# Kernel tuning notes

Measured on AMD Instinct MI355X. Metric: run time of the kernel, lower is better.

The kernel has to match this reference:

```python
import jax, jax.numpy as jnp
import numpy as np
from functools import partial

B, T, D, H, HL, L, C = 64, 1024, 256, 256, 256, 2, 128


def _rnn_layer(x, Wih, Whh, bih, bhh):
    # x: [B, T, D] -> outputs [B, T, H]; torch nn.RNN (tanh) semantics
    proj = jnp.einsum('btd,hd->bth', x, Wih) + bih + bhh  # precompute input projection
    h0 = jnp.zeros((x.shape[0], Whh.shape[0]), x.dtype)

    def step(h, p_t):
        h = jnp.tanh(p_t + h @ Whh.T)
        return h, h

    _, ys = jax.lax.scan(step, h0, proj.swapaxes(0, 1))  # scan over time [T, B, H]
    return ys.swapaxes(0, 1)


def _lstm_layer(x, Wih, Whh, bih, bhh):
    # torch nn.LSTM gate order: i, f, g, o. Wih: [4H, D], Whh: [4H, H]
    Hh = Whh.shape[1]
    proj = jnp.einsum('btd,gd->btg', x, Wih) + bih + bhh  # [B, T, 4H]
    h0 = jnp.zeros((x.shape[0], Hh), x.dtype)
    c0 = jnp.zeros((x.shape[0], Hh), x.dtype)

    def step(carry, p_t):
        h, c = carry
        gates = p_t + h @ Whh.T
        i, f, g, o = jnp.split(gates, 4, axis=-1)
        i = jax.nn.sigmoid(i)
        f = jax.nn.sigmoid(f)
        g = jnp.tanh(g)
        o = jax.nn.sigmoid(o)
        c = f * c + i * g
        h = o * jnp.tanh(c)
        return (h, c), h

    _, ys = jax.lax.scan(step, (h0, c0), proj.swapaxes(0, 1))
    return ys.swapaxes(0, 1)


def setup_inputs() -> dict:
    key = jax.random.key(0)
    ks = jax.random.split(key, 12)
    s = 1.0 / np.sqrt(H)
    return {
        'rnn_x': jax.random.normal(ks[0], (B, T, D), jnp.float32),
        'lstm_x': jax.random.normal(ks[1], (B, T, D), jnp.float32),
        'rnn_Wih': jax.random.normal(ks[2], (L, H, D), jnp.float32) * s,
        'rnn_Whh': jax.random.normal(ks[3], (L, H, H), jnp.float32) * s,
        'rnn_bih': jax.random.normal(ks[4], (L, H), jnp.float32) * s,
        'rnn_bhh': jax.random.normal(ks[5], (L, H), jnp.float32) * s,
        'lstm_Wih': jax.random.normal(ks[6], (L, 4 * HL, D), jnp.float32) * s,
        'lstm_Whh': jax.random.normal(ks[7], (L, 4 * HL, HL), jnp.float32) * s,
        'lstm_bih': jax.random.normal(ks[8], (L, 4 * HL), jnp.float32) * s,
        'lstm_bhh': jax.random.normal(ks[9], (L, 4 * HL), jnp.float32) * s,
        'fc_W': jax.random.normal(ks[10], (C, H + HL), jnp.float32) * (1.0 / np.sqrt(H + HL)),
        'fc_b': jax.random.normal(ks[11], (C,), jnp.float32) * (1.0 / np.sqrt(H + HL)),
    }


def reference(rnn_x, lstm_x, rnn_Wih, rnn_Whh, rnn_bih, rnn_bhh,
              lstm_Wih, lstm_Whh, lstm_bih, lstm_bhh, fc_W, fc_b):
    r = rnn_x
    for l in range(L):
        r = _rnn_layer(r, rnn_Wih[l], rnn_Whh[l], rnn_bih[l], rnn_bhh[l])
    m = lstm_x
    for l in range(L):
        m = _lstm_layer(m, lstm_Wih[l], lstm_Whh[l], lstm_bih[l], lstm_bhh[l])
    feat = jnp.concatenate([r[:, -1, :], m[:, -1, :]], axis=1)  # [B, H+HL]
    return feat @ fc_W.T + fc_b
```

## Files before the change

kernel.cpp:

```cpp
#include <hip/hip_runtime.h>
#include <stdint.h>

#define T_ 1024

typedef short bf16x8 __attribute__((ext_vector_type(8)));
typedef float f32x4  __attribute__((ext_vector_type(4)));
typedef unsigned short u16;

#define MFMA(a,b,c) __builtin_amdgcn_mfma_f32_16x16x32_bf16((a),(b),(c),0,0,0)

__device__ __forceinline__ u16 f2bf(float f){
  unsigned u = __float_as_uint(f);
  return (u16)((u + 0x7FFFu + ((u>>16)&1u)) >> 16);
}
__device__ __forceinline__ float bf2f(u16 s){ return __uint_as_float(((unsigned)s)<<16); }
__device__ __forceinline__ float sigm(float x){ return 1.f/(1.f+__expf(-x)); }
__device__ __forceinline__ float tanhq(float x){ return 2.f/(1.f+__expf(-2.f*x)) - 1.f; }

__device__ __forceinline__ void gload16(const void* g, void* l){
  __builtin_amdgcn_global_load_lds(
      (const __attribute__((address_space(1))) unsigned int*)g,
      (__attribute__((address_space(3)))       unsigned int*)l, 16, 0, 0);
}
__device__ __forceinline__ void lgkm0_barrier(){
  asm volatile("s_waitcnt lgkmcnt(0)" ::: "memory");
  __builtin_amdgcn_s_barrier();
  asm volatile("" ::: "memory");
}

__global__ void k_cvt(const float* __restrict__ s, u16* __restrict__ d, int n4){
  int i = blockIdx.x*blockDim.x + threadIdx.x;
  int stride = gridDim.x*blockDim.x;
  for (; i < n4; i += stride){
    float4 v = ((const float4*)s)[i];
    ushort4 o; o.x=f2bf(v.x); o.y=f2bf(v.y); o.z=f2bf(v.z); o.w=f2bf(v.w);
    ((ushort4*)d)[i] = o;
  }
}

__global__ __launch_bounds__(256,2) void k_gemm(
    const u16* __restrict__ A, const u16* __restrict__ Bm,
    u16* __restrict__ C, int N)
{
  __shared__ u16 As[128*64];
  __shared__ u16 Bs[128*64];
  const int tid = threadIdx.x;
  const int lane = tid & 63, w = tid >> 6;
  const int l15 = lane & 15, l4 = lane >> 4;
  const long m0 = (long)blockIdx.x * 128;
  const int  n0 = blockIdx.y * 128;
  const int  mo = (w>>1)*64, no = (w&1)*64;

  f32x4 acc[4][4];
  #pragma unroll
  for (int i=0;i<4;++i)
    #pragma unroll
    for (int j=0;j<4;++j) acc[i][j] = (f32x4){0.f,0.f,0.f,0.f};

  for (int kt=0; kt<4; ++kt){
    const int k0 = kt*64;
    #pragma unroll
    for (int i=0;i<4;++i){
      int fb = (i*256+tid)*16;
      int r  = fb>>7, cbyte = fb&127;
      gload16(A + (m0 + r)*256 + k0 + (cbyte>>1), (char*)As + fb);
      gload16(Bm + (long)(n0 + r)*256 + k0 + (cbyte>>1), (char*)Bs + fb);
    }
    __syncthreads();
    #pragma unroll
    for (int kb=0;kb<2;++kb){
      bf16x8 a[4], b[4];
      #pragma unroll
      for (int mb=0;mb<4;++mb)
        a[mb] = *(const bf16x8*)(As + (mo+mb*16+l15)*64 + kb*32 + l4*8);
      #pragma unroll
      for (int nb=0;nb<4;++nb)
        b[nb] = *(const bf16x8*)(Bs + (no+nb*16+l15)*64 + kb*32 + l4*8);
      #pragma unroll
      for (int mb=0;mb<4;++mb)
        #pragma unroll
        for (int nb=0;nb<4;++nb)
          acc[mb][nb] = MFMA(a[mb], b[nb], acc[mb][nb]);
    }
    __syncthreads();
  }
  #pragma unroll
  for (int mb=0;mb<4;++mb)
    #pragma unroll
    for (int nb=0;nb<4;++nb)
      #pragma unroll
      for (int j=0;j<4;++j){
        long row = m0 + mo + mb*16 + l4*4 + j;
        int  col = n0 + no + nb*16 + l15;
        C[row*N + col] = f2bf(acc[mb][nb][j]);
      }
}

__global__ __launch_bounds__(512,2) void k_rec(
    const u16*  __restrict__ projR,
    const float* __restrict__ WhhR,
    const float* __restrict__ bihR, const float* __restrict__ bhhR,
    u16* __restrict__ yR,
    const u16*  __restrict__ projL,
    const float* __restrict__ WhhL,
    const float* __restrict__ bihL, const float* __restrict__ bhhL,
    u16* __restrict__ yL,
    u16* __restrict__ hbuf,
    int* __restrict__ flags,
    float* __restrict__ feat,
    int lastMode)
{
  __shared__ u16 hlds[16*256];
  const int tid = threadIdx.x;
  const int lane = tid & 63, w = tid >> 6;
  const int l15 = lane & 15, l4 = lane >> 4, l7 = lane & 7;
  const int bid = blockIdx.x;

  if (bid < 4){
    const int g = bid;
    const int cb = 32*w;
    bf16x8 bhi[2][8], blo[2][8];
    #pragma unroll
    for (int nb=0;nb<2;++nb){
      const int col = cb + nb*16 + l15;
      #pragma unroll
      for (int kb=0;kb<8;++kb){
        const float* wp = WhhR + (long)col*256 + kb*32 + l4*8;
        #pragma unroll
        for (int j=0;j<8;++j){
          float wv = wp[j];
          u16 hi = f2bf(wv);
          bhi[nb][kb][j] = (short)hi;
          blo[nb][kb][j] = (short)f2bf(wv - bf2f(hi));
        }
      }
    }
    float bias[2];
    #pragma unroll
    for (int nb=0;nb<2;++nb){ int col = cb+nb*16+l15; bias[nb]=bihR[col]+bhhR[col]; }

    u16 pfr[8];
    #pragma unroll
    for (int nb=0;nb<2;++nb)
      #pragma unroll
      for (int j=0;j<4;++j)
        pfr[nb*4+j] = projR[((long)(16*g + l4*4 + j)*T_ + 0)*256 + cb + nb*16 + l15];

    for (int t=0; t<T_; ++t){
      lgkm0_barrier();
      f32x4 acc0 = {0.f,0.f,0.f,0.f}, acc1 = acc0;
      if (t > 0){
        bf16x8 a[8];
        #pragma unroll
        for (int kb=0;kb<8;++kb){
          int bo = (l15*512 + kb*64 + l4*16) ^ ((l15&7)<<4);
          a[kb] = *(const bf16x8*)((const char*)hlds + bo);
        }
        #pragma unroll
        for (int kb=0;kb<8;++kb){
          acc0 = MFMA(a[kb], bhi[0][kb], acc0);
          acc0 = MFMA(a[kb], blo[0][kb], acc0);
          acc1 = MFMA(a[kb], bhi[1][kb], acc1);
          acc1 = MFMA(a[kb], blo[1][kb], acc1);
        }
      }
      float hv[2][4];
      #pragma unroll
      for (int nb=0;nb<2;++nb)
        #pragma unroll
        for (int j=0;j<4;++j){
          float pre = (nb ? acc1[j] : acc0[j]) + bf2f(pfr[nb*4+j]) + bias[nb];
          hv[nb][j] = tanhq(pre);
        }
      int tn = (t+1 < T_) ? t+1 : t;
      #pragma unroll
      for (int nb=0;nb<2;++nb)
        #pragma unroll
        for (int j=0;j<4;++j)
          pfr[nb*4+j] = projR[((long)(16*g + l4*4 + j)*T_ + tn)*256 + cb + nb*16 + l15];
      lgkm0_barrier();
      #pragma unroll
      for (int nb=0;nb<2;++nb)
        #pragma unroll
        for (int j=0;j<4;++j){
          int m = l4*4 + j, u = cb + nb*16 + l15;
          u16 hb = f2bf(hv[nb][j]);
          int bo = (m*512 + u*2) ^ ((m&7)<<4);
          *(u16*)((char*)hlds + bo) = hb;
          if (yR) yR[((long)(16*g+m)*T_ + t)*256 + u] = hb;
          if (lastMode && t == T_-1) feat[(16*g+m)*512 + u] = hv[nb][j];
        }
    }
  } else {
    const int wg = bid - 4;
    const int bg = wg >> 2, hg = wg & 3;
    const int ub = 64*hg + 8*w;
    const int ugl = ub + l7;
    bf16x8 bhi[2][8], blo[2][8];
    float bias[2];
    #pragma unroll
    for (int nb=0;nb<2;++nb){
      const int gate = nb*2 + (l15>>3);
      const long wr = (long)(gate*256 + ub + l7);
      bias[nb] = bihL[wr] + bhhL[wr];
      #pragma unroll
      for (int kb=0;kb<8;++kb){
        const float* wp = WhhL + wr*256 + kb*32 + l4*8;
        #pragma unroll
        for (int j=0;j<8;++j){
          float wv = wp[j];
          u16 hi = f2bf(wv);
          bhi[nb][kb][j] = (short)hi;
          blo[nb][kb][j] = (short)f2bf(wv - bf2f(hi));
        }
      }
    }
    u16 pfr[8];
    #pragma unroll
    for (int nb=0;nb<2;++nb){
      const int gate = nb*2 + (l15>>3);
      #pragma unroll
      for (int j=0;j<4;++j)
        pfr[nb*4+j] = projL[((long)(16*bg + l4*4 + j)*T_ + 0)*1024 + gate*256 + ub + l7];
    }
    float c4[4] = {0.f,0.f,0.f,0.f};
    const bool lowHalf = ((lane & 8) == 0);

    for (int t=0; t<T_; ++t){
      const int par = t & 1, pn = par ^ 1;
      if (t > 0 && tid == 0){
        while (__hip_atomic_load(flags + bg, __ATOMIC_RELAXED, __HIP_MEMORY_SCOPE_AGENT) < 4*t)
          __builtin_amdgcn_s_sleep(1);
        __threadfence();
      }
      lgkm0_barrier();
      f32x4 acc0 = {0.f,0.f,0.f,0.f}, acc1 = acc0;
      if (t > 0){
        bf16x8 a[8];
        const u16* hb = hbuf + par*16384 + (16*bg + l15)*256;
        #pragma unroll
        for (int kb=0;kb<8;++kb) a[kb] = *(const bf16x8*)(hb + kb*32 + l4*8);
        #pragma unroll
        for (int kb=0;kb<8;++kb){
          acc0 = MFMA(a[kb], bhi[0][kb], acc0);
          acc0 = MFMA(a[kb], blo[0][kb], acc0);
          acc1 = MFMA(a[kb], bhi[1][kb], acc1);
          acc1 = MFMA(a[kb], blo[1][kb], acc1);
        }
      }
      #pragma unroll
      for (int j=0;j<4;++j){
        float s0 = acc0[j] + bf2f(pfr[j])   + bias[0];
        float s1 = acc1[j] + bf2f(pfr[4+j]) + bias[1];
        float g0 = sigm(s0);
        float g1 = lowHalf ? tanhq(s1) : sigm(s1);
        float p0 = __shfl_xor(g0, 8);
        float p1 = __shfl_xor(g1, 8);
        float iv = lowHalf ? g0 : p0;
        float fv = lowHalf ? p0 : g0;
        float gv = lowHalf ? g1 : p1;
        float ov = lowHalf ? p1 : g1;
        float cv = fv * c4[j] + iv * gv;
        c4[j] = cv;
        float hval = ov * tanhq(cv);
        int m = l4*4 + j;
        if (lowHalf){
          u16 hb2 = f2bf(hval);
          hbuf[pn*16384 + (16*bg+m)*256 + ugl] = hb2;
          if (yL) yL[((long)(16*bg+m)*T_ + t)*256 + ugl] = hb2;
          if (lastMode && t == T_-1) feat[(16*bg+m)*512 + 256 + ugl] = hval;
        }
      }
      int tn = (t+1 < T_) ? t+1 : t;
      #pragma unroll
      for (int nb=0;nb<2;++nb){
        const int gate = nb*2 + (l15>>3);
        #pragma unroll
        for (int j=0;j<4;++j)
          pfr[nb*4+j] = projL[((long)(16*bg + l4*4 + j)*T_ + tn)*1024 + gate*256 + ub + l7];
      }
      asm volatile("s_waitcnt vmcnt(8)" ::: "memory");
      __builtin_amdgcn_s_barrier();
      asm volatile("" ::: "memory");
      if (tid == 0){ __threadfence(); atomicAdd(flags + bg, 1); }
    }
  }
}

__global__ void k_fc(const float* __restrict__ feat, const float* __restrict__ W,
                     const float* __restrict__ bias, float* __restrict__ out){
  int o = blockIdx.x*blockDim.x + threadIdx.x;
  if (o >= 64*128) return;
  int b = o >> 7, c = o & 127;
  float s = bias[c];
  const float* f  = feat + b*512;
  const float* wr = W + c*512;
  #pragma unroll 8
  for (int k=0;k<512;++k) s += f[k]*wr[k];
  out[o] = s;
}

extern "C" void kernel_launch(void* const* d_in, const int* in_sizes, int n_in,
                              void* d_out, int out_size, void* d_ws, size_t ws_size,
                              hipStream_t stream)
{
  (void)in_sizes; (void)n_in; (void)out_size; (void)ws_size;
  const float* rnn_x    = (const float*)d_in[0];
  const float* lstm_x   = (const float*)d_in[1];
  const float* rnn_Wih  = (const float*)d_in[2];
  const float* rnn_Whh  = (const float*)d_in[3];
  const float* rnn_bih  = (const float*)d_in[4];
  const float* rnn_bhh  = (const float*)d_in[5];
  const float* lstm_Wih = (const float*)d_in[6];
  const float* lstm_Whh = (const float*)d_in[7];
  const float* lstm_bih = (const float*)d_in[8];
  const float* lstm_bhh = (const float*)d_in[9];
  const float* fc_W     = (const float*)d_in[10];
  const float* fc_b     = (const float*)d_in[11];
  float* out = (float*)d_out;

  char* ws = (char*)d_ws; size_t off = 0;
  auto alloc = [&](size_t b)->char*{ char* p = ws + off; off += (b + 255) & ~(size_t)255; return p; };
  const size_t NE = (size_t)64*1024*256;
  u16*  wih_r = (u16*)alloc(2*256*256*2);
  u16*  wih_l = (u16*)alloc(2*1024*256*2);
  u16*  xr    = (u16*)alloc(NE*2);
  u16*  xl    = (u16*)alloc(NE*2);
  u16*  projR = (u16*)alloc(NE*2);
  u16*  projL = (u16*)alloc(NE*4*2);
  u16*  hbuf  = (u16*)alloc(2*64*256*2);
  int*  flags = (int*)alloc(256);
  float* feat = (float*)alloc(64*512*4);

  hipMemsetAsync(flags, 0, 256, stream);
  k_cvt<<<2048,256,0,stream>>>(rnn_x,  xr, (int)(NE/4));
  k_cvt<<<2048,256,0,stream>>>(lstm_x, xl, (int)(NE/4));
  k_cvt<<<64, 256,0,stream>>>(rnn_Wih,  wih_r, 2*256*256/4);
  k_cvt<<<256,256,0,stream>>>(lstm_Wih, wih_l, 2*1024*256/4);
  k_gemm<<<dim3(512,2),256,0,stream>>>(xr, wih_r, projR, 256);
  k_gemm<<<dim3(512,8),256,0,stream>>>(xl, wih_l, projL, 1024);
  k_rec<<<20,512,0,stream>>>(projR, rnn_Whh, rnn_bih, rnn_bhh, xr,
                             projL, lstm_Whh, lstm_bih, lstm_bhh, xl,
                             hbuf, flags, nullptr, 0);
  k_gemm<<<dim3(512,2),256,0,stream>>>(xr, wih_r + 256*256,  projR, 256);
  k_gemm<<<dim3(512,8),256,0,stream>>>(xl, wih_l + 1024*256, projL, 1024);
  k_rec<<<20,512,0,stream>>>(projR, rnn_Whh + 256*256, rnn_bih + 256, rnn_bhh + 256, nullptr,
                             projL, lstm_Whh + 1024*256, lstm_bih + 1024, lstm_bhh + 1024, nullptr,
                             hbuf, flags + 32, feat, 1);
  k_fc<<<32,256,0,stream>>>(feat, fc_W, fc_b, out);
}
```

Measured before the change: 10.69 ms.

## Shrink LSTM recurrence to four blocks with per-wave flags and cache-bypass loads

The LSTM part of the recurrent kernel now uses 4 workgroups, one per hidden slice, and each walks all four batch groups instead of using one workgroup per batch/hidden pair. The block-wide barrier plus atomic counter is replaced with per-wave flag words written and polled through coherent (sc0 sc1) global stores and loads. Loads of the next batch group's h fragments are overlapped with the MFMAs of the current one. The aim is to cut the number of participants in each step's cross-block handshake and the barrier cost, at the price of more serial work per block and hand-written waitcnt ordering that is fragile.

```diff
diff --git a/kernel.cpp b/kernel.cpp
--- a/kernel.cpp
+++ b/kernel.cpp
@@ -27,6 +27,32 @@
   __builtin_amdgcn_s_barrier();
   asm volatile("" ::: "memory");
 }
+
+__device__ __forceinline__ int coh_ld32(const int* p){
+  int r;
+  asm volatile("global_load_dword %0, %1, off sc0 sc1\n\ts_waitcnt vmcnt(0)"
+               : "=v"(r) : "v"(p) : "memory");
+  return r;
+}
+__device__ __forceinline__ void coh_st32(int* p, int v){
+  asm volatile("global_store_dword %0, %1, off sc0 sc1" :: "v"(p), "v"(v) : "memory");
+}
+__device__ __forceinline__ void coh_st16(u16* p, u16 v){
+  unsigned vv = v;
+  asm volatile("global_store_short %0, %1, off sc0 sc1" :: "v"(p), "v"(vv) : "memory");
+}
+__device__ __forceinline__ void coh_ld_frags(const u16* base, bf16x8 a[8]){
+  asm volatile("global_load_dwordx4 %0, %1, off sc0 sc1"            : "=v"(a[0]) : "v"(base) : "memory");
+  asm volatile("global_load_dwordx4 %0, %1, off offset:64 sc0 sc1"  : "=v"(a[1]) : "v"(base) : "memory");
+  asm volatile("global_load_dwordx4 %0, %1, off offset:128 sc0 sc1" : "=v"(a[2]) : "v"(base) : "memory");
+  asm volatile("global_load_dwordx4 %0, %1, off offset:192 sc0 sc1" : "=v"(a[3]) : "v"(base) : "memory");
+  asm volatile("global_load_dwordx4 %0, %1, off offset:256 sc0 sc1" : "=v"(a[4]) : "v"(base) : "memory");
+  asm volatile("global_load_dwordx4 %0, %1, off offset:320 sc0 sc1" : "=v"(a[5]) : "v"(base) : "memory");
+  asm volatile("global_load_dwordx4 %0, %1, off offset:384 sc0 sc1" : "=v"(a[6]) : "v"(base) : "memory");
+  asm volatile("global_load_dwordx4 %0, %1, off offset:448 sc0 sc1" : "=v"(a[7]) : "v"(base) : "memory");
+}
+#define VMCNT(n) do{ asm volatile("s_waitcnt vmcnt(" #n ")" ::: "memory"); \
+                     __builtin_amdgcn_sched_barrier(0); }while(0)
 
 __global__ void k_cvt(const float* __restrict__ s, u16* __restrict__ d, int n4){
   int i = blockIdx.x*blockDim.x + threadIdx.x;
@@ -115,6 +141,7 @@
   const int lane = tid & 63, w = tid >> 6;
   const int l15 = lane & 15, l4 = lane >> 4, l7 = lane & 7;
   const int bid = blockIdx.x;
+  (void)lastMode;
 
   if (bid < 4){
     const int g = bid;
@@ -188,12 +215,11 @@
           int bo = (m*512 + u*2) ^ ((m&7)<<4);
           *(u16*)((char*)hlds + bo) = hb;
           if (yR) yR[((long)(16*g+m)*T_ + t)*256 + u] = hb;
-          if (lastMode && t == T_-1) feat[(16*g+m)*512 + u] = hv[nb][j];
+          if (feat && t == T_-1) feat[(16*g+m)*512 + u] = hv[nb][j];
         }
     }
   } else {
-    const int wg = bid - 4;
-    const int bg = wg >> 2, hg = wg & 3;
+    const int hg = bid - 4;
     const int ub = 64*hg + 8*w;
     const int ugl = ub + l7;
     bf16x8 bhi[2][8], blo[2][8];
@@ -201,7 +227,7 @@
     #pragma unroll
     for (int nb=0;nb<2;++nb){
       const int gate = nb*2 + (l15>>3);
-      const long wr = (long)(gate*256 + ub + l7);
+      const long wr = (long)(gate*256 + ugl);
       bias[nb] = bihL[wr] + bhhL[wr];
       #pragma unroll
       for (int kb=0;kb<8;++kb){
@@ -215,74 +241,83 @@
         }
       }
     }
-    u16 pfr[8];
-    #pragma unroll
-    for (int nb=0;nb<2;++nb){
-      const int gate = nb*2 + (l15>>3);
-      #pragma unroll
-      for (int j=0;j<4;++j)
-        pfr[nb*4+j] = projL[((long)(16*bg + l4*4 + j)*T_ + 0)*1024 + gate*256 + ub + l7];
-    }
-    float c4[4] = {0.f,0.f,0.f,0.f};
+    u16 pfr[4][8];
+    #pragma unroll
+    for (int bg=0;bg<4;++bg)
+      #pragma unroll
+      for (int nb=0;nb<2;++nb){
+        const int gate = nb*2 + (l15>>3);
+        #pragma unroll
+        for (int j=0;j<4;++j)
+          pfr[bg][nb*4+j] = projL[((long)(16*bg + l4*4 + j)*T_ + 0)*1024 + gate*256 + ugl];
+      }
+    float cst[4][4];
+    #pragma unroll
+    for (int bg=0;bg<4;++bg){ cst[bg][0]=0.f;cst[bg][1]=0.f;cst[bg][2]=0.f;cst[bg][3]=0.f; }
     const bool lowHalf = ((lane & 8) == 0);
+    int* flg = flags;
 
     for (int t=0; t<T_; ++t){
       const int par = t & 1, pn = par ^ 1;
-      if (t > 0 && tid == 0){
-        while (__hip_atomic_load(flags + bg, __ATOMIC_RELAXED, __HIP_MEMORY_SCOPE_AGENT) < 4*t)
-          __builtin_amdgcn_s_sleep(1);
-        __threadfence();
-      }
-      lgkm0_barrier();
-      f32x4 acc0 = {0.f,0.f,0.f,0.f}, acc1 = acc0;
+      bf16x8 afr[8];
       if (t > 0){
-        bf16x8 a[8];
-        const u16* hb = hbuf + par*16384 + (16*bg + l15)*256;
-        #pragma unroll
-        for (int kb=0;kb<8;++kb) a[kb] = *(const bf16x8*)(hb + kb*32 + l4*8);
-        #pragma unroll
-        for (int kb=0;kb<8;++kb){
-          acc0 = MFMA(a[kb], bhi[0][kb], acc0);
-          acc0 = MFMA(a[kb], blo[0][kb], acc0);
-          acc1 = MFMA(a[kb], bhi[1][kb], acc1);
-          acc1 = MFMA(a[kb], blo[1][kb], acc1);
-        }
-      }
-      #pragma unroll
-      for (int j=0;j<4;++j){
-        float s0 = acc0[j] + bf2f(pfr[j])   + bias[0];
-        float s1 = acc1[j] + bf2f(pfr[4+j]) + bias[1];
-        float g0 = sigm(s0);
-        float g1 = lowHalf ? tanhq(s1) : sigm(s1);
-        float p0 = __shfl_xor(g0, 8);
-        float p1 = __shfl_xor(g1, 8);
-        float iv = lowHalf ? g0 : p0;
-        float fv = lowHalf ? p0 : g0;
-        float gv = lowHalf ? g1 : p1;
-        float ov = lowHalf ? p1 : g1;
-        float cv = fv * c4[j] + iv * gv;
-        c4[j] = cv;
-        float hval = ov * tanhq(cv);
-        int m = l4*4 + j;
-        if (lowHalf){
-          u16 hb2 = f2bf(hval);
-          hbuf[pn*16384 + (16*bg+m)*256 + ugl] = hb2;
-          if (yL) yL[((long)(16*bg+m)*T_ + t)*256 + ugl] = hb2;
-          if (lastMode && t == T_-1) feat[(16*bg+m)*512 + 256 + ugl] = hval;
-        }
-      }
-      int tn = (t+1 < T_) ? t+1 : t;
-      #pragma unroll
-      for (int nb=0;nb<2;++nb){
-        const int gate = nb*2 + (l15>>3);
-        #pragma unroll
-        for (int j=0;j<4;++j)
-          pfr[nb*4+j] = projL[((long)(16*bg + l4*4 + j)*T_ + tn)*1024 + gate*256 + ub + l7];
+        while (true){
+          int a0 = coh_ld32(flg + lane);
+          int a1 = coh_ld32(flg + 64 + lane);
+          if (__all((a0 >= t) & (a1 >= t))) break;
+          __builtin_amdgcn_s_sleep(2);
+        }
+        coh_ld_frags(hbuf + par*16384 + l15*256 + l4*8, afr);
+      }
+      #pragma unroll
+      for (int bg=0;bg<4;++bg){
+        f32x4 acc0={0.f,0.f,0.f,0.f}, acc1={0.f,0.f,0.f,0.f};
+        if (t > 0){
+          if (bg == 0){ VMCNT(0); } else { VMCNT(12); }
+          #pragma unroll
+          for (int kb=0;kb<8;++kb){
+            acc0 = MFMA(afr[kb], bhi[0][kb], acc0);
+            acc0 = MFMA(afr[kb], blo[0][kb], acc0);
+            acc1 = MFMA(afr[kb], bhi[1][kb], acc1);
+            acc1 = MFMA(afr[kb], blo[1][kb], acc1);
+          }
+          if (bg < 3)
+            coh_ld_frags(hbuf + par*16384 + (16*(bg+1)+l15)*256 + l4*8, afr);
+        }
+        #pragma unroll
+        for (int j=0;j<4;++j){
+          float s0 = acc0[j] + bf2f(pfr[bg][j])   + bias[0];
+          float s1 = acc1[j] + bf2f(pfr[bg][4+j]) + bias[1];
+          float g0 = sigm(s0);
+          float g1 = lowHalf ? tanhq(s1) : sigm(s1);
+          float p0 = __shfl_xor(g0, 8);
+          float p1 = __shfl_xor(g1, 8);
+          float iv = lowHalf ? g0 : p0;
+          float fv = lowHalf ? p0 : g0;
+          float gv = lowHalf ? g1 : p1;
+          float ov = lowHalf ? p1 : g1;
+          float cv = fv * cst[bg][j] + iv * gv;
+          cst[bg][j] = cv;
+          float hval = ov * tanhq(cv);
+          const int m = 16*bg + l4*4 + j;
+          if (lowHalf){
+            u16 hb2 = f2bf(hval);
+            coh_st16(hbuf + pn*16384 + m*256 + ugl, hb2);
+            if (yL) yL[((long)m*T_ + t)*256 + ugl] = hb2;
+            if (feat && t == T_-1) feat[m*512 + 256 + ugl] = hval;
+          }
+        }
+        const int tn = (t+1 < T_) ? t+1 : t;
+        #pragma unroll
+        for (int nb=0;nb<2;++nb){
+          const int gate = nb*2 + (l15>>3);
+          #pragma unroll
+          for (int j=0;j<4;++j)
+            pfr[bg][nb*4+j] = projL[((long)(16*bg + l4*4 + j)*T_ + tn)*1024 + gate*256 + ugl];
+        }
       }
       asm volatile("s_waitcnt vmcnt(8)" ::: "memory");
-      __builtin_amdgcn_s_barrier();
-      asm volatile("" ::: "memory");
-      if (tid == 0){ __threadfence(); atomicAdd(flags + bg, 1); }
+      if (lane < 4) coh_st32(flg + lane*32 + hg*8 + w, t+1);
     }
   }
 }
@@ -329,23 +364,23 @@
   u16*  projR = (u16*)alloc(NE*2);
   u16*  projL = (u16*)alloc(NE*4*2);
   u16*  hbuf  = (u16*)alloc(2*64*256*2);
-  int*  flags = (int*)alloc(256);
+  int*  flags = (int*)alloc(1024);
   float* feat = (float*)alloc(64*512*4);
 
-  hipMemsetAsync(flags, 0, 256, stream);
+  hipMemsetAsync(flags, 0, 1024, stream);
   k_cvt<<<2048,256,0,stream>>>(rnn_x,  xr, (int)(NE/4));
   k_cvt<<<2048,256,0,stream>>>(lstm_x, xl, (int)(NE/4));
   k_cvt<<<64, 256,0,stream>>>(rnn_Wih,  wih_r, 2*256*256/4);
   k_cvt<<<256,256,0,stream>>>(lstm_Wih, wih_l, 2*1024*256/4);
   k_gemm<<<dim3(512,2),256,0,stream>>>(xr, wih_r, projR, 256);
   k_gemm<<<dim3(512,8),256,0,stream>>>(xl, wih_l, projL, 1024);
-  k_rec<<<20,512,0,stream>>>(projR, rnn_Whh, rnn_bih, rnn_bhh, xr,
-                             projL, lstm_Whh, lstm_bih, lstm_bhh, xl,
-                             hbuf, flags, nullptr, 0);
+  k_rec<<<8,512,0,stream>>>(projR, rnn_Whh, rnn_bih, rnn_bhh, xr,
+                            projL, lstm_Whh, lstm_bih, lstm_bhh, xl,
+                            hbuf, flags, nullptr, 0);
   k_gemm<<<dim3(512,2),256,0,stream>>>(xr, wih_r + 256*256,  projR, 256);
   k_gemm<<<dim3(512,8),256,0,stream>>>(xl, wih_l + 1024*256, projL, 1024);
-  k_rec<<<20,512,0,stream>>>(projR, rnn_Whh + 256*256, rnn_bih + 256, rnn_bhh + 256, nullptr,
-                             projL, lstm_Whh + 1024*256, lstm_bih + 1024, lstm_bhh + 1024, nullptr,
-                             hbuf, flags + 32, feat, 1);
+  k_rec<<<8,512,0,stream>>>(projR, rnn_Whh + 256*256, rnn_bih + 256, rnn_bhh + 256, nullptr,
+                            projL, lstm_Whh + 1024*256, lstm_bih + 1024, lstm_bhh + 1024, nullptr,
+                            hbuf, flags + 128, feat, 1);
   k_fc<<<32,256,0,stream>>>(feat, fc_W, fc_b, out);
 }
```

After: 36.53 ms. 242% more time.

## Replace LSTM atomic flag sync with tagged h-buffer polling and batch-interleaved pipeline

Applied to the files above, without the earlier changes.

The LSTM recurrence shrinks from 16 to 4 workgroups. Each workgroup now owns a hidden-unit slice for all four batch groups and interleaves them so one group's exchange latency hides behind another group's compute. The atomic counter barrier is replaced by a tag (layer, batch group, timestep) packed into the upper half of each h word. Consumers poll with uncached loads until the tags match. The GEMM output layout changes to time-major so per-step projection reads are contiguous. This trades fewer global round-trips for more work per workgroup and depends on the polling being correct.

```diff
diff --git a/kernel.cpp b/kernel.cpp
--- a/kernel.cpp
+++ b/kernel.cpp
@@ -5,6 +5,7 @@
 
 typedef short bf16x8 __attribute__((ext_vector_type(8)));
 typedef float f32x4  __attribute__((ext_vector_type(4)));
+typedef int   i32x4  __attribute__((ext_vector_type(4)));
 typedef unsigned short u16;
 
 #define MFMA(a,b,c) __builtin_amdgcn_mfma_f32_16x16x32_bf16((a),(b),(c),0,0,0)
@@ -27,6 +28,12 @@
   __builtin_amdgcn_s_barrier();
   asm volatile("" ::: "memory");
 }
+
+#define VMCNT(n) do{ asm volatile("s_waitcnt vmcnt(" #n ")" ::: "memory"); \
+                     __builtin_amdgcn_sched_barrier(0); }while(0)
+#define LD_X4(dst, p, OFF) asm volatile("global_load_dwordx4 %0, %1, off offset:" #OFF " sc0 sc1" : "=v"(dst) : "v"(p) : "memory")
+#define ST_TAG(p, v)       asm volatile("global_store_dword %0, %1, off sc0 sc1" :: "v"(p), "v"(v) : "memory")
+#define LD_U16(dst, p, OFF) asm volatile("global_load_ushort %0, %1, off offset:" #OFF : "=v"(dst) : "v"(p) : "memory")
 
 __global__ void k_cvt(const float* __restrict__ s, u16* __restrict__ d, int n4){
   int i = blockIdx.x*blockDim.x + threadIdx.x;
@@ -90,9 +97,10 @@
     for (int nb=0;nb<4;++nb)
       #pragma unroll
       for (int j=0;j<4;++j){
-        long row = m0 + mo + mb*16 + l4*4 + j;
+        long m   = m0 + mo + mb*16 + l4*4 + j;
+        long crow= (long)(m & 1023)*64 + (m >> 10);
         int  col = n0 + no + nb*16 + l15;
-        C[row*N + col] = f2bf(acc[mb][nb][j]);
+        C[crow*N + col] = f2bf(acc[mb][nb][j]);
       }
 }
 
@@ -105,12 +113,12 @@
     const float* __restrict__ WhhL,
     const float* __restrict__ bihL, const float* __restrict__ bhhL,
     u16* __restrict__ yL,
-    u16* __restrict__ hbuf,
-    int* __restrict__ flags,
+    unsigned* __restrict__ hbuf,
     float* __restrict__ feat,
-    int lastMode)
+    int lay)
 {
   __shared__ u16 hlds[16*256];
+  __shared__ u16 lsm[2*16*256];
   const int tid = threadIdx.x;
   const int lane = tid & 63, w = tid >> 6;
   const int l15 = lane & 15, l4 = lane >> 4, l7 = lane & 7;
@@ -144,7 +152,7 @@
     for (int nb=0;nb<2;++nb)
       #pragma unroll
       for (int j=0;j<4;++j)
-        pfr[nb*4+j] = projR[((long)(16*g + l4*4 + j)*T_ + 0)*256 + cb + nb*16 + l15];
+        pfr[nb*4+j] = projR[(long)(0*64 + 16*g + l4*4 + j)*256 + cb + nb*16 + l15];
 
     for (int t=0; t<T_; ++t){
       lgkm0_barrier();
@@ -177,7 +185,7 @@
       for (int nb=0;nb<2;++nb)
         #pragma unroll
         for (int j=0;j<4;++j)
-          pfr[nb*4+j] = projR[((long)(16*g + l4*4 + j)*T_ + tn)*256 + cb + nb*16 + l15];
+          pfr[nb*4+j] = projR[(long)(tn*64 + 16*g + l4*4 + j)*256 + cb + nb*16 + l15];
       lgkm0_barrier();
       #pragma unroll
       for (int nb=0;nb<2;++nb)
@@ -188,20 +196,25 @@
           int bo = (m*512 + u*2) ^ ((m&7)<<4);
           *(u16*)((char*)hlds + bo) = hb;
           if (yR) yR[((long)(16*g+m)*T_ + t)*256 + u] = hb;
-          if (lastMode && t == T_-1) feat[(16*g+m)*512 + u] = hv[nb][j];
+          if (feat && t == T_-1) feat[(16*g+m)*512 + u] = hv[nb][j];
         }
     }
   } else {
-    const int wg = bid - 4;
-    const int bg = wg >> 2, hg = wg & 3;
+    const int hg = bid - 4;
     const int ub = 64*hg + 8*w;
     const int ugl = ub + l7;
+    const int srow  = 2*w + (lane>>5);
+    const int scol8 = (lane&31)*8;
+    const int swro  = ((srow*512 + (lane&31)*16) ^ ((srow&7)<<4));
+    char* lsmBE = (char*)lsm;
+    char* lsmBO = (char*)lsm + 8192;
+
     bf16x8 bhi[2][8], blo[2][8];
     float bias[2];
     #pragma unroll
     for (int nb=0;nb<2;++nb){
       const int gate = nb*2 + (l15>>3);
-      const long wr = (long)(gate*256 + ub + l7);
+      const long wr = (long)(gate*256 + ugl);
       bias[nb] = bihL[wr] + bhhL[wr];
       #pragma unroll
       for (int kb=0;kb<8;++kb){
@@ -215,75 +228,115 @@
         }
       }
     }
-    u16 pfr[8];
-    #pragma unroll
-    for (int nb=0;nb<2;++nb){
-      const int gate = nb*2 + (l15>>3);
-      #pragma unroll
-      for (int j=0;j<4;++j)
-        pfr[nb*4+j] = projL[((long)(16*bg + l4*4 + j)*T_ + 0)*1024 + gate*256 + ub + l7];
-    }
-    float c4[4] = {0.f,0.f,0.f,0.f};
+    float cst[4][4];
+    #pragma unroll
+    for (int b_=0;b_<4;++b_){ cst[b_][0]=0.f;cst[b_][1]=0.f;cst[b_][2]=0.f;cst[b_][3]=0.f; }
     const bool lowHalf = ((lane & 8) == 0);
-
-    for (int t=0; t<T_; ++t){
-      const int par = t & 1, pn = par ^ 1;
-      if (t > 0 && tid == 0){
-        while (__hip_atomic_load(flags + bg, __ATOMIC_RELAXED, __HIP_MEMORY_SCOPE_AGENT) < 4*t)
-          __builtin_amdgcn_s_sleep(1);
-        __threadfence();
-      }
-      lgkm0_barrier();
-      f32x4 acc0 = {0.f,0.f,0.f,0.f}, acc1 = acc0;
-      if (t > 0){
-        bf16x8 a[8];
-        const u16* hb = hbuf + par*16384 + (16*bg + l15)*256;
-        #pragma unroll
-        for (int kb=0;kb<8;++kb) a[kb] = *(const bf16x8*)(hb + kb*32 + l4*8);
-        #pragma unroll
-        for (int kb=0;kb<8;++kb){
-          acc0 = MFMA(a[kb], bhi[0][kb], acc0);
-          acc0 = MFMA(a[kb], blo[0][kb], acc0);
-          acc1 = MFMA(a[kb], bhi[1][kb], acc1);
-          acc1 = MFMA(a[kb], blo[1][kb], acc1);
-        }
-      }
-      #pragma unroll
-      for (int j=0;j<4;++j){
-        float s0 = acc0[j] + bf2f(pfr[j])   + bias[0];
-        float s1 = acc1[j] + bf2f(pfr[4+j]) + bias[1];
-        float g0 = sigm(s0);
-        float g1 = lowHalf ? tanhq(s1) : sigm(s1);
-        float p0 = __shfl_xor(g0, 8);
-        float p1 = __shfl_xor(g1, 8);
-        float iv = lowHalf ? g0 : p0;
-        float fv = lowHalf ? p0 : g0;
-        float gv = lowHalf ? g1 : p1;
-        float ov = lowHalf ? p1 : g1;
-        float cv = fv * c4[j] + iv * gv;
-        c4[j] = cv;
-        float hval = ov * tanhq(cv);
-        int m = l4*4 + j;
-        if (lowHalf){
-          u16 hb2 = f2bf(hval);
-          hbuf[pn*16384 + (16*bg+m)*256 + ugl] = hb2;
-          if (yL) yL[((long)(16*bg+m)*T_ + t)*256 + ugl] = hb2;
-          if (lastMode && t == T_-1) feat[(16*bg+m)*512 + 256 + ugl] = hval;
-        }
-      }
-      int tn = (t+1 < T_) ? t+1 : t;
-      #pragma unroll
-      for (int nb=0;nb<2;++nb){
-        const int gate = nb*2 + (l15>>3);
-        #pragma unroll
-        for (int j=0;j<4;++j)
-          pfr[nb*4+j] = projL[((long)(16*bg + l4*4 + j)*T_ + tn)*1024 + gate*256 + ub + l7];
-      }
-      asm volatile("s_waitcnt vmcnt(8)" ::: "memory");
-      __builtin_amdgcn_s_barrier();
-      asm volatile("" ::: "memory");
-      if (tid == 0){ __threadfence(); atomicAdd(flags + bg, 1); }
-    }
+    i32x4 rE0, rE1, rO0, rO1;
+    unsigned pfE[8], pfO[8];
+
+    #define PFR_ISSUE(PF, TP, BGP) do{                                             \
+      const u16* pb  = projL + ((size_t)((TP)*64 + 16*(BGP) + l4*4)*1024 + (l15>>3)*256 + ugl); \
+      const u16* pb2 = pb + 2048;                                                  \
+      LD_U16(PF[0], pb, 0);    LD_U16(PF[4], pb, 1024);                            \
+      LD_U16(PF[1], pb, 2048); LD_U16(PF[5], pb, 3072);                            \
+      LD_U16(PF[2], pb2, 0);    LD_U16(PF[6], pb2, 1024);                          \
+      LD_U16(PF[3], pb2, 2048); LD_U16(PF[7], pb2, 3072);                          \
+    }while(0)
+
+    #define STAGE_ISSUE(R0, R1, T2, BG2) do{                                       \
+      const unsigned* sp = hbuf + ((T2)&1)*16384 + (16*(BG2) + srow)*256 + scol8;  \
+      LD_X4(R0, sp, 0); LD_X4(R1, sp, 16);                                         \
+    }while(0)
+
+    #define LACT(BG, PF, TT) do{                                                   \
+      const unsigned tws = (unsigned)(((lay<<13)|((BG)<<11)|((TT)+1))<<16);        \
+      unsigned* hstb = hbuf + (((TT)&1)^1)*16384 + (16*(BG) + l4*4)*256 + ugl;     \
+      _Pragma("unroll")                                                            \
+      for (int j=0;j<4;++j){                                                       \
+        float s0v = acc0[j] + bf2f((u16)PF[j])   + bias[0];                        \
+        float s1v = acc1[j] + bf2f((u16)PF[4+j]) + bias[1];                        \
+        float g0 = sigm(s0v);                                                      \
+        float g1 = lowHalf ? tanhq(s1v) : sigm(s1v);                               \
+        float p0 = __shfl_xor(g0, 8);                                              \
+        float p1 = __shfl_xor(g1, 8);                                              \
+        float iv = lowHalf ? g0 : p0;                                              \
+        float fv = lowHalf ? p0 : g0;                                              \
+        float gv = lowHalf ? g1 : p1;                                              \
+        float ov = lowHalf ? p1 : g1;                                              \
+        float cv = fv * cst[BG][j] + iv * gv;                                      \
+        cst[BG][j] = cv;                                                           \
+        float hval = ov * tanhq(cv);                                               \
+        if (lowHalf){                                                              \
+          u16 hb2 = f2bf(hval);                                                    \
+          unsigned dw = tws | (unsigned)hb2;                                       \
+          ST_TAG(hstb + j*256, dw);                                                \
+          yL[((long)(16*(BG) + l4*4 + j)*T_ + (TT))*256 + ugl] = hb2;              \
+          if (feat && (TT) == T_-1) feat[(16*(BG)+l4*4+j)*512 + 256 + ugl] = hval; \
+        }                                                                          \
+      }                                                                            \
+    }while(0)
+
+    PFR_ISSUE(pfE, 0, 0);
+    PFR_ISSUE(pfO, 0, 1);
+    VMCNT(0);
+    {
+      f32x4 acc0 = {0.f,0.f,0.f,0.f}, acc1 = {0.f,0.f,0.f,0.f};
+      LACT(0, pfE, 0); PFR_ISSUE(pfE, 0, 2);
+      LACT(1, pfO, 0); PFR_ISSUE(pfO, 0, 3);
+      STAGE_ISSUE(rE0, rE1, 1, 0); VMCNT(0);
+      LACT(2, pfE, 0); PFR_ISSUE(pfE, 1, 0);
+      STAGE_ISSUE(rO0, rO1, 1, 1); VMCNT(0);
+      LACT(3, pfO, 0); PFR_ISSUE(pfO, 1, 1);
+    }
+
+    #define LSLOT(BG, R0, R1, PF, LSB) do{                                         \
+      VMCNT(34);                                                                   \
+      {                                                                            \
+        const unsigned tw = (unsigned)(((lay<<13)|((BG)<<11)|t)<<16);              \
+        for(;;){                                                                   \
+          unsigned bad;                                                            \
+          bad  = (unsigned)(R0[0]^(int)tw)&0xFFFF0000u;                            \
+          bad |= (unsigned)(R0[1]^(int)tw)&0xFFFF0000u;                            \
+          bad |= (unsigned)(R0[2]^(int)tw)&0xFFFF0000u;                            \
+          bad |= (unsigned)(R0[3]^(int)tw)&0xFFFF0000u;                            \
+          bad |= (unsigned)(R1[0]^(int)tw)&0xFFFF0000u;                            \
+          bad |= (unsigned)(R1[1]^(int)tw)&0xFFFF0000u;                            \
+          bad |= (unsigned)(R1[2]^(int)tw)&0xFFFF0000u;                            \
+          bad |= (unsigned)(R1[3]^(int)tw)&0xFFFF0000u;                            \
+          if (!__any(bad != 0u)) break;                                            \
+          STAGE_ISSUE(R0, R1, t, BG); VMCNT(0);                                    \
+        }                                                                          \
+        i32x4 pk;                                                                  \
+        pk[0]=(int)__builtin_amdgcn_perm((unsigned)R0[1],(unsigned)R0[0],0x05040100u); \
+        pk[1]=(int)__builtin_amdgcn_perm((unsigned)R0[3],(unsigned)R0[2],0x05040100u); \
+        pk[2]=(int)__builtin_amdgcn_perm((unsigned)R1[1],(unsigned)R1[0],0x05040100u); \
+        pk[3]=(int)__builtin_amdgcn_perm((unsigned)R1[3],(unsigned)R1[2],0x05040100u); \
+        *(i32x4*)(lsmB##LSB + swro) = pk;                                          \
+      }                                                                            \
+      { int t2 = t + ((BG)>=2 ? 1:0); if (t2 > T_-1) t2 = T_-1;                    \
+        STAGE_ISSUE(R0, R1, t2, ((BG)+2)&3); }                                     \
+      lgkm0_barrier();                                                             \
+      f32x4 acc0 = {0.f,0.f,0.f,0.f}, acc1 = {0.f,0.f,0.f,0.f};                    \
+      _Pragma("unroll")                                                            \
+      for (int kb=0;kb<8;++kb){                                                    \
+        bf16x8 a = *(const bf16x8*)(lsmB##LSB + ((l15*512 + kb*64 + l4*16) ^ ((l15&7)<<4))); \
+        acc0 = MFMA(a, bhi[0][kb], acc0);  acc0 = MFMA(a, blo[0][kb], acc0);       \
+        acc1 = MFMA(a, bhi[1][kb], acc1);  acc1 = MFMA(a, blo[1][kb], acc1);       \
+      }                                                                            \
+      VMCNT(20);                                                                   \
+      LACT(BG, PF, t);                                                             \
+      { int tp = t + ((BG)>=2 ? 1:0); if (tp > T_-1) tp = T_-1;                    \
+        PFR_ISSUE(PF, tp, ((BG)+2)&3); }                                           \
+    }while(0)
+
+    for (int t=1; t<T_; ++t){
+      LSLOT(0, rE0, rE1, pfE, E);
+      LSLOT(1, rO0, rO1, pfO, O);
+      LSLOT(2, rE0, rE1, pfE, E);
+      LSLOT(3, rO0, rO1, pfO, O);
+    }
+    VMCNT(0);
   }
 }
 
@@ -328,24 +381,22 @@
   u16*  xl    = (u16*)alloc(NE*2);
   u16*  projR = (u16*)alloc(NE*2);
   u16*  projL = (u16*)alloc(NE*4*2);
-  u16*  hbuf  = (u16*)alloc(2*64*256*2);
-  int*  flags = (int*)alloc(256);
+  unsigned* hbuf = (unsigned*)alloc(2*64*256*4);
   float* feat = (float*)alloc(64*512*4);
 
-  hipMemsetAsync(flags, 0, 256, stream);
   k_cvt<<<2048,256,0,stream>>>(rnn_x,  xr, (int)(NE/4));
   k_cvt<<<2048,256,0,stream>>>(lstm_x, xl, (int)(NE/4));
   k_cvt<<<64, 256,0,stream>>>(rnn_Wih,  wih_r, 2*256*256/4);
   k_cvt<<<256,256,0,stream>>>(lstm_Wih, wih_l, 2*1024*256/4);
   k_gemm<<<dim3(512,2),256,0,stream>>>(xr, wih_r, projR, 256);
   k_gemm<<<dim3(512,8),256,0,stream>>>(xl, wih_l, projL, 1024);
-  k_rec<<<20,512,0,stream>>>(projR, rnn_Whh, rnn_bih, rnn_bhh, xr,
-                             projL, lstm_Whh, lstm_bih, lstm_bhh, xl,
-                             hbuf, flags, nullptr, 0);
+  k_rec<<<8,512,0,stream>>>(projR, rnn_Whh, rnn_bih, rnn_bhh, xr,
+                            projL, lstm_Whh, lstm_bih, lstm_bhh, xl,
+                            hbuf, nullptr, 0);
   k_gemm<<<dim3(512,2),256,0,stream>>>(xr, wih_r + 256*256,  projR, 256);
   k_gemm<<<dim3(512,8),256,0,stream>>>(xl, wih_l + 1024*256, projL, 1024);
-  k_rec<<<20,512,0,stream>>>(projR, rnn_Whh + 256*256, rnn_bih + 256, rnn_bhh + 256, nullptr,
-                             projL, lstm_Whh + 1024*256, lstm_bih + 1024, lstm_bhh + 1024, nullptr,
-                             hbuf, flags + 32, feat, 1);
+  k_rec<<<8,512,0,stream>>>(projR, rnn_Whh + 256*256, rnn_bih + 256, rnn_bhh + 256, nullptr,
+                            projL, lstm_Whh + 1024*256, lstm_bih + 1024, lstm_bhh + 1024, xl,
+                            hbuf, feat, 1);
   k_fc<<<32,256,0,stream>>>(feat, fc_W, fc_b, out);
 }
```

New measurement: 21.60 ms. +102.1%, slower.

## Replace LSTM counter-flag barrier with per-element tagged hidden-state polling

Applied to the files above, without the earlier changes.

The cross-block LSTM recurrence stops using an atomic counter flag plus a spin by one thread and a block barrier. Each hidden value is now stored as a 32-bit word that carries a layer/timestep tag in its upper half. Consumers poll their own fragment loads with cache-bypassing loads until every tag matches, then unpack the bf16 values with perm for the MFMA. The next step's fragment loads are issued early to overlap with the gate math. This removes the atomic round-trip and the block barrier from the critical path, but doubles the hidden-state traffic and can trigger repeated reloads while waiting.

```diff
diff --git a/kernel.cpp b/kernel.cpp
--- a/kernel.cpp
+++ b/kernel.cpp
@@ -5,6 +5,7 @@
 
 typedef short bf16x8 __attribute__((ext_vector_type(8)));
 typedef float f32x4  __attribute__((ext_vector_type(4)));
+typedef int   i32x4  __attribute__((ext_vector_type(4)));
 typedef unsigned short u16;
 
 #define MFMA(a,b,c) __builtin_amdgcn_mfma_f32_16x16x32_bf16((a),(b),(c),0,0,0)
@@ -27,6 +28,11 @@
   __builtin_amdgcn_s_barrier();
   asm volatile("" ::: "memory");
 }
+
+#define VMCNT0 do{ asm volatile("s_waitcnt vmcnt(0)" ::: "memory"); \
+                   __builtin_amdgcn_sched_barrier(0); }while(0)
+#define LD_FR(dst,p,OFF)  asm volatile("global_load_dwordx4 %0, %1, off offset:" #OFF " sc0 sc1" : "=v"(dst) : "v"(p) : "memory")
+#define ST_DWO(p,v,OFF)   asm volatile("global_store_dword %0, %1, off offset:" #OFF " sc0 sc1" :: "v"(p), "v"(v) : "memory")
 
 __global__ void k_cvt(const float* __restrict__ s, u16* __restrict__ d, int n4){
   int i = blockIdx.x*blockDim.x + threadIdx.x;
@@ -105,10 +111,9 @@
     const float* __restrict__ WhhL,
     const float* __restrict__ bihL, const float* __restrict__ bhhL,
     u16* __restrict__ yL,
-    u16* __restrict__ hbuf,
-    int* __restrict__ flags,
+    unsigned* __restrict__ hbuf,
     float* __restrict__ feat,
-    int lastMode)
+    int lay)
 {
   __shared__ u16 hlds[16*256];
   const int tid = threadIdx.x;
@@ -188,7 +193,7 @@
           int bo = (m*512 + u*2) ^ ((m&7)<<4);
           *(u16*)((char*)hlds + bo) = hb;
           if (yR) yR[((long)(16*g+m)*T_ + t)*256 + u] = hb;
-          if (lastMode && t == T_-1) feat[(16*g+m)*512 + u] = hv[nb][j];
+          if (lay && t == T_-1) feat[(16*g+m)*512 + u] = hv[nb][j];
         }
     }
   } else {
@@ -201,7 +206,7 @@
     #pragma unroll
     for (int nb=0;nb<2;++nb){
       const int gate = nb*2 + (l15>>3);
-      const long wr = (long)(gate*256 + ub + l7);
+      const long wr = (long)(gate*256 + ugl);
       bias[nb] = bihL[wr] + bhhL[wr];
       #pragma unroll
       for (int kb=0;kb<8;++kb){
@@ -221,33 +226,60 @@
       const int gate = nb*2 + (l15>>3);
       #pragma unroll
       for (int j=0;j<4;++j)
-        pfr[nb*4+j] = projL[((long)(16*bg + l4*4 + j)*T_ + 0)*1024 + gate*256 + ub + l7];
+        pfr[nb*4+j] = projL[((long)(16*bg + l4*4 + j)*T_ + 0)*1024 + gate*256 + ugl];
     }
     float c4[4] = {0.f,0.f,0.f,0.f};
     const bool lowHalf = ((lane & 8) == 0);
+    const size_t loff = (size_t)(16*bg + l15)*256 + (size_t)l4*8;
+    i32x4 FR[16];
+
+    #define FRISSUE(FB) do{                                            \
+      LD_FR(FR[0],(FB),0);    LD_FR(FR[1],(FB),16);                    \
+      LD_FR(FR[2],(FB),128);  LD_FR(FR[3],(FB),144);                   \
+      LD_FR(FR[4],(FB),256);  LD_FR(FR[5],(FB),272);                   \
+      LD_FR(FR[6],(FB),384);  LD_FR(FR[7],(FB),400);                   \
+      LD_FR(FR[8],(FB),512);  LD_FR(FR[9],(FB),528);                   \
+      LD_FR(FR[10],(FB),640); LD_FR(FR[11],(FB),656);                  \
+      LD_FR(FR[12],(FB),768); LD_FR(FR[13],(FB),784);                  \
+      LD_FR(FR[14],(FB),896); LD_FR(FR[15],(FB),912);                  \
+    }while(0)
 
     for (int t=0; t<T_; ++t){
-      const int par = t & 1, pn = par ^ 1;
-      if (t > 0 && tid == 0){
-        while (__hip_atomic_load(flags + bg, __ATOMIC_RELAXED, __HIP_MEMORY_SCOPE_AGENT) < 4*t)
+      f32x4 acc0 = {0.f,0.f,0.f,0.f}, acc1 = {0.f,0.f,0.f,0.f};
+      if (t > 0){
+        const unsigned tw = (unsigned)(((lay<<11)|t)<<16);
+        const unsigned* fb = hbuf + (size_t)((t-1)&1)*16384 + loff;
+        VMCNT0;
+        for(;;){
+          unsigned bad = 0u;
+          #pragma unroll
+          for (int r=0;r<16;++r){
+            bad |= ((unsigned)FR[r][0] ^ tw) & 0xFFFF0000u;
+            bad |= ((unsigned)FR[r][1] ^ tw) & 0xFFFF0000u;
+            bad |= ((unsigned)FR[r][2] ^ tw) & 0xFFFF0000u;
+            bad |= ((unsigned)FR[r][3] ^ tw) & 0xFFFF0000u;
+          }
+          if (!__any(bad != 0u)) break;
           __builtin_amdgcn_s_sleep(1);
-        __threadfence();
-      }
-      lgkm0_barrier();
-      f32x4 acc0 = {0.f,0.f,0.f,0.f}, acc1 = acc0;
-      if (t > 0){
-        bf16x8 a[8];
-        const u16* hb = hbuf + par*16384 + (16*bg + l15)*256;
-        #pragma unroll
-        for (int kb=0;kb<8;++kb) a[kb] = *(const bf16x8*)(hb + kb*32 + l4*8);
+          FRISSUE(fb);
+          VMCNT0;
+        }
         #pragma unroll
         for (int kb=0;kb<8;++kb){
-          acc0 = MFMA(a[kb], bhi[0][kb], acc0);
-          acc0 = MFMA(a[kb], blo[0][kb], acc0);
-          acc1 = MFMA(a[kb], bhi[1][kb], acc1);
-          acc1 = MFMA(a[kb], blo[1][kb], acc1);
-        }
-      }
+          i32x4 p;
+          p[0]=(int)__builtin_amdgcn_perm((unsigned)FR[2*kb][1],  (unsigned)FR[2*kb][0],  0x05040100u);
+          p[1]=(int)__builtin_amdgcn_perm((unsigned)FR[2*kb][3],  (unsigned)FR[2*kb][2],  0x05040100u);
+          p[2]=(int)__builtin_amdgcn_perm((unsigned)FR[2*kb+1][1],(unsigned)FR[2*kb+1][0],0x05040100u);
+          p[3]=(int)__builtin_amdgcn_perm((unsigned)FR[2*kb+1][3],(unsigned)FR[2*kb+1][2],0x05040100u);
+          bf16x8 a = *(bf16x8*)&p;
+          acc0 = MFMA(a, bhi[0][kb], acc0);
+          acc0 = MFMA(a, blo[0][kb], acc0);
+          acc1 = MFMA(a, bhi[1][kb], acc1);
+          acc1 = MFMA(a, blo[1][kb], acc1);
+        }
+      }
+      const unsigned tst = (unsigned)(((lay<<11)|(t+1))<<16);
+      unsigned* sb = hbuf + (size_t)(t&1)*16384 + (size_t)(16*bg + l4*4)*256 + ugl;
       #pragma unroll
       for (int j=0;j<4;++j){
         float s0 = acc0[j] + bf2f(pfr[j])   + bias[0];
@@ -263,13 +295,14 @@
         float cv = fv * c4[j] + iv * gv;
         c4[j] = cv;
         float hval = ov * tanhq(cv);
-        int m = l4*4 + j;
+        int m = 16*bg + l4*4 + j;
         if (lowHalf){
           u16 hb2 = f2bf(hval);
-          hbuf[pn*16384 + (16*bg+m)*256 + ugl] = hb2;
-          if (yL) yL[((long)(16*bg+m)*T_ + t)*256 + ugl] = hb2;
-          if (lastMode && t == T_-1) feat[(16*bg+m)*512 + 256 + ugl] = hval;
-        }
+          ST_DWO(sb, tst | (unsigned)hb2, 0);
+          if (yL) yL[((long)m*T_ + t)*256 + ugl] = hb2;
+          if (lay && t == T_-1) feat[m*512 + 256 + ugl] = hval;
+        }
+        sb += 256;
       }
       int tn = (t+1 < T_) ? t+1 : t;
       #pragma unroll
@@ -277,13 +310,14 @@
         const int gate = nb*2 + (l15>>3);
         #pragma unroll
         for (int j=0;j<4;++j)
-          pfr[nb*4+j] = projL[((long)(16*bg + l4*4 + j)*T_ + tn)*1024 + gate*256 + ub + l7];
-      }
-      asm volatile("s_waitcnt vmcnt(8)" ::: "memory");
-      __builtin_amdgcn_s_barrier();
-      asm volatile("" ::: "memory");
-      if (tid == 0){ __threadfence(); atomicAdd(flags + bg, 1); }
-    }
+          pfr[nb*4+j] = projL[((long)(16*bg + l4*4 + j)*T_ + tn)*1024 + gate*256 + ugl];
+      }
+      if (t+1 < T_){
+        const unsigned* fb2 = hbuf + (size_t)(t&1)*16384 + loff;
+        FRISSUE(fb2);
+      }
+    }
+    VMCNT0;
   }
 }
 
@@ -328,11 +362,10 @@
   u16*  xl    = (u16*)alloc(NE*2);
   u16*  projR = (u16*)alloc(NE*2);
   u16*  projL = (u16*)alloc(NE*4*2);
-  u16*  hbuf  = (u16*)alloc(2*64*256*2);
-  int*  flags = (int*)alloc(256);
+  unsigned* hbuf = (unsigned*)alloc(2*64*256*4);
   float* feat = (float*)alloc(64*512*4);
 
-  hipMemsetAsync(flags, 0, 256, stream);
+  hipMemsetAsync(hbuf, 0, 2*64*256*4, stream);
   k_cvt<<<2048,256,0,stream>>>(rnn_x,  xr, (int)(NE/4));
   k_cvt<<<2048,256,0,stream>>>(lstm_x, xl, (int)(NE/4));
   k_cvt<<<64, 256,0,stream>>>(rnn_Wih,  wih_r, 2*256*256/4);
@@ -341,11 +374,11 @@
   k_gemm<<<dim3(512,8),256,0,stream>>>(xl, wih_l, projL, 1024);
   k_rec<<<20,512,0,stream>>>(projR, rnn_Whh, rnn_bih, rnn_bhh, xr,
                              projL, lstm_Whh, lstm_bih, lstm_bhh, xl,
-                             hbuf, flags, nullptr, 0);
+                             hbuf, feat, 0);
   k_gemm<<<dim3(512,2),256,0,stream>>>(xr, wih_r + 256*256,  projR, 256);
   k_gemm<<<dim3(512,8),256,0,stream>>>(xl, wih_l + 1024*256, projL, 1024);
   k_rec<<<20,512,0,stream>>>(projR, rnn_Whh + 256*256, rnn_bih + 256, rnn_bhh + 256, nullptr,
                              projL, lstm_Whh + 1024*256, lstm_bih + 1024, lstm_bhh + 1024, nullptr,
-                             hbuf, flags + 32, feat, 1);
+                             hbuf, feat, 1);
   k_fc<<<32,256,0,stream>>>(feat, fc_W, fc_b, out);
 }
```

After: 34.92 ms. 3.27x slower.
